# Kernel tuning notes

Measured on AMD Instinct MI355X. Metric: run time of the kernel, lower is better.

Reference implementation:

```python
import jax, jax.numpy as jnp
import numpy as np

H = 64  # hidden_dim

def _lstm_dir(x, Wih, Whh, bih, bhh, reverse):
    # x: [B, T, D]; Wih: [4H, D]; Whh: [4H, H]; PyTorch gate order i,f,g,o
    B, T, _ = x.shape
    if reverse:
        x = x[:, ::-1, :]
    # Precompute input contribution to all gates: [B, T, 4H]
    xg = jnp.einsum('btd,gd->btg', x, Wih) + (bih + bhh)
    h0 = jnp.zeros((B, H), x.dtype)
    c0 = jnp.zeros((B, H), x.dtype)

    def step(carry, xg_t):
        h, c = carry
        g = xg_t + h @ Whh.T  # [B, 4H]
        i, f, gg, o = jnp.split(g, 4, axis=-1)
        i = jax.nn.sigmoid(i)
        f = jax.nn.sigmoid(f)
        gg = jnp.tanh(gg)
        o = jax.nn.sigmoid(o)
        c = f * c + i * gg
        h = o * jnp.tanh(c)
        return (h, c), h

    (hT, cT), hs = jax.lax.scan(step, (h0, c0), jnp.swapaxes(xg, 0, 1))
    hs = jnp.swapaxes(hs, 0, 1)  # [B, T, H]
    if reverse:
        hs = hs[:, ::-1, :]
    return hs, hT

def _forward(x, Wih_l0_f, Whh_l0_f, bih_l0_f, bhh_l0_f,
             Wih_l0_b, Whh_l0_b, bih_l0_b, bhh_l0_b,
             Wih_l1_f, Whh_l1_f, bih_l1_f, bhh_l1_f,
             Wih_l1_b, Whh_l1_b, bih_l1_b, bhh_l1_b,
             fc1_W, fc1_b, fc2_W, fc2_b):
    xt = jnp.transpose(x, (0, 2, 1))  # [B, 512, 3]
    # Layer 0 (bidirectional)
    hs_f, _ = _lstm_dir(xt, Wih_l0_f, Whh_l0_f, bih_l0_f, bhh_l0_f, False)
    hs_b, _ = _lstm_dir(xt, Wih_l0_b, Whh_l0_b, bih_l0_b, bhh_l0_b, True)
    y0 = jnp.concatenate([hs_f, hs_b], axis=-1)  # [B, 512, 2H]
    # (inter-layer dropout is identity in eval mode)
    # Layer 1 (bidirectional); only final hidden states needed
    _, hT_f = _lstm_dir(y0, Wih_l1_f, Whh_l1_f, bih_l1_f, bhh_l1_f, False)
    _, hT_b = _lstm_dir(y0, Wih_l1_b, Whh_l1_b, bih_l1_b, bhh_l1_b, True)
    h = jnp.concatenate([hT_f, hT_b], axis=-1)  # [B, 2H]
    h = jax.nn.relu(h @ fc1_W.T + fc1_b)
    return h @ fc2_W.T + fc2_b  # [B, num_classes]

def setup_inputs() -> dict:
    key = jax.random.key(0)
    ks = iter(jax.random.split(key, 32))
    B, T, C = 1024, 512, 3
    d = {}
    d['x'] = jax.random.normal(next(ks), (B, C, T), dtype=jnp.float32)
    # PyTorch-style bias init: forget-gate bias = 1, rest 0
    bias = jnp.zeros((4 * H,), jnp.float32).at[H:2 * H].set(1.0)
    for layer, din in [(0, C), (1, 2 * H)]:
        for dirn in ['f', 'b']:
            d[f'Wih_l{layer}_{dirn}'] = jax.random.normal(next(ks), (4 * H, din), dtype=jnp.float32) * 0.1
            d[f'Whh_l{layer}_{dirn}'] = jax.random.normal(next(ks), (4 * H, H), dtype=jnp.float32) * 0.1
            d[f'bih_l{layer}_{dirn}'] = bias
            d[f'bhh_l{layer}_{dirn}'] = jnp.zeros((4 * H,), jnp.float32)
    d['fc1_W'] = jax.random.normal(next(ks), (H, 2 * H), dtype=jnp.float32) * 0.1
    d['fc1_b'] = jnp.zeros((H,), jnp.float32)
    d['fc2_W'] = jax.random.normal(next(ks), (2, H), dtype=jnp.float32) * 0.1
    d['fc2_b'] = jnp.zeros((2,), jnp.float32)
    return d

def reference(x, Wih_l0_f, Whh_l0_f, bih_l0_f, bhh_l0_f,
              Wih_l0_b, Whh_l0_b, bih_l0_b, bhh_l0_b,
              Wih_l1_f, Whh_l1_f, bih_l1_f, bhh_l1_f,
              Wih_l1_b, Whh_l1_b, bih_l1_b, bhh_l1_b,
              fc1_W, fc1_b, fc2_W, fc2_b):
    return _forward(x, Wih_l0_f, Whh_l0_f, bih_l0_f, bhh_l0_f,
                    Wih_l0_b, Whh_l0_b, bih_l0_b, bhh_l0_b,
                    Wih_l1_f, Whh_l1_f, bih_l1_f, bhh_l1_f,
                    Wih_l1_b, Whh_l1_b, bih_l1_b, bhh_l1_b,
                    fc1_W, fc1_b, fc2_W, fc2_b)
```

## Files before the change

kernel.cpp:

```cpp
#include <hip/hip_runtime.h>
#include <stdint.h>

typedef __attribute__((ext_vector_type(8))) short short8;
typedef __attribute__((ext_vector_type(4))) float f32x4;

#define TT 512
#define LSTR 136
#define XS 516

static __device__ __forceinline__ uint32_t f2bf_u(float f){
  union { float f; uint32_t u; } v; v.f = f;
  return (v.u + 0x7fffu + ((v.u >> 16) & 1u)) >> 16;
}
static __device__ __forceinline__ short8 w8f32(const float* p){
  float4 a = *(const float4*)p;
  float4 b = *(const float4*)(p + 4);
  short8 r;
  r[0] = (short)f2bf_u(a.x); r[1] = (short)f2bf_u(a.y);
  r[2] = (short)f2bf_u(a.z); r[3] = (short)f2bf_u(a.w);
  r[4] = (short)f2bf_u(b.x); r[5] = (short)f2bf_u(b.y);
  r[6] = (short)f2bf_u(b.z); r[7] = (short)f2bf_u(b.w);
  return r;
}
static __device__ __forceinline__ float sigx(float x){
  float e = __builtin_amdgcn_exp2f(-1.442695040888963f * x);
  return __builtin_amdgcn_rcpf(1.f + e);
}
static __device__ __forceinline__ float tanhx(float x){
  float e = __builtin_amdgcn_exp2f(-2.885390081777927f * x);
  return fmaf(__builtin_amdgcn_rcpf(1.f + e), 2.f, -1.f);
}
static __device__ __forceinline__ void lds_barrier(){
  asm volatile("s_waitcnt lgkmcnt(0)" ::: "memory");
  __builtin_amdgcn_s_barrier();
}
#define MF(A,B,C) __builtin_amdgcn_mfma_f32_16x16x32_bf16((A),(B),(C),0,0,0)

#define NONLIN_WRITE(A0V, A1V, P1) do { \
    float g0_ = sel0 ? (A0V)[0] : (A1V)[0]; \
    float g1_ = sel0 ? (A0V)[1] : (A1V)[1]; \
    float g2_ = sel0 ? (A0V)[2] : (A1V)[2]; \
    float g3_ = sel0 ? (A0V)[3] : (A1V)[3]; \
    float ii_ = sigx(g0_), ff_ = sigx(g1_), gg_ = tanhx(g2_), oo_ = sigx(g3_); \
    c = fmaf(ff_, c, ii_ * gg_); \
    h = oo_ * tanhx(c); \
    sZ[P1][m8][colw] = (unsigned short)f2bf_u(h); \
  } while(0)

__global__ __launch_bounds__(512, 2) void lstm_l0(
    const float* __restrict__ x,
    const float* __restrict__ Wih_f, const float* __restrict__ Whh_f,
    const float* __restrict__ bih_f, const float* __restrict__ bhh_f,
    const float* __restrict__ Wih_b, const float* __restrict__ Whh_b,
    const float* __restrict__ bih_b, const float* __restrict__ bhh_b,
    unsigned short* __restrict__ y0)
{
  const int tid = threadIdx.x;
  const int wv = tid >> 6, lane = tid & 63;
  const int quad = lane >> 4, m16 = lane & 15;
  const int dir = blockIdx.y;
  const int bbase = blockIdx.x * 8;
  const float* Wih = dir ? Wih_b : Wih_f;
  const float* Whh = dir ? Whh_b : Whh_f;
  const float* bih = dir ? bih_b : bih_f;
  const float* bhh = dir ? bhh_b : bhh_f;

  __shared__ __align__(16) unsigned short sZ[2][8][LSTR];
  __shared__ __align__(16) float sX[24 * XS];

  short8 aH[2][2];
  f32x4 biasv[2];
  float Wf[2][4][3];
  const int gm = (m16 & 3) * 64 + (m16 >> 2);
  #pragma unroll
  for (int i = 0; i < 2; i++){
    const int rt = 2 * wv + i;
    const int g = gm + 4 * rt;
    aH[i][0] = w8f32(Whh + g * 64 + quad * 8);
    aH[i][1] = w8f32(Whh + g * 64 + 32 + quad * 8);
    const int gu = 4 * rt + quad;
    #pragma unroll
    for (int r = 0; r < 4; r++){
      biasv[i][r] = bih[r * 64 + gu] + bhh[r * 64 + gu];
      #pragma unroll
      for (int d = 0; d < 3; d++) Wf[i][r][d] = Wih[(r * 64 + gu) * 3 + d];
    }
  }

  for (int idx = tid; idx < 2 * 8 * LSTR; idx += 512)
    ((unsigned short*)sZ)[idx] = 0;
  for (int i4 = tid; i4 < 3072; i4 += 512){
    const int row = i4 >> 7, t4 = (i4 & 127) * 4;
    *(float4*)&sX[row * XS + t4] = *(const float4*)(x + (size_t)bbase * 1536 + row * 512 + t4);
  }
  __syncthreads();

  const int m8 = m16 & 7;
  const int xrow = 3 * m8;
  const bool sel0 = (m16 < 8);
  const int colw = 8 * wv + quad + ((m16 >> 3) << 2);
  float c = 0.f, h = 0.f;

#define FFCOMP(F0, F1, TIDX) do { \
    float x0_ = sX[xrow * XS + (TIDX)]; \
    float x1_ = sX[(xrow + 1) * XS + (TIDX)]; \
    float x2_ = sX[(xrow + 2) * XS + (TIDX)]; \
    _Pragma("unroll") \
    for (int r_ = 0; r_ < 4; r_++){ \
      F0[r_] = fmaf(Wf[0][r_][2], x2_, fmaf(Wf[0][r_][1], x1_, fmaf(Wf[0][r_][0], x0_, biasv[0][r_]))); \
      F1[r_] = fmaf(Wf[1][r_][2], x2_, fmaf(Wf[1][r_][1], x1_, fmaf(Wf[1][r_][0], x0_, biasv[1][r_]))); \
    } \
  } while(0)

  f32x4 FBa0, FBa1, FBb0, FBb1;
  {
    const int t0_ = dir ? (TT - 1) : 0;
    FFCOMP(FBa0, FBa1, t0_);
  }

#define L0STEP(S, P, FC0, FC1, FN0, FN1) do { \
    const int p1_ = (P) ^ 1; \
    short8 bh0 = *(const short8*)&sZ[P][m8][     quad * 8]; \
    short8 bh1 = *(const short8*)&sZ[P][m8][32 + quad * 8]; \
    if (lane < 8 && (S) > 0){ \
      const int tprev = dir ? (TT - (S)) : ((S) - 1); \
      uint4 v_ = *(const uint4*)&sZ[P][wv][lane * 8]; \
      *(uint4*)(y0 + ((size_t)(bbase + wv) * TT + tprev) * 128 + dir * 64 + lane * 8) = v_; \
    } \
    f32x4 A0 = MF(aH[0][0], bh0, FC0); \
    f32x4 A1 = MF(aH[1][0], bh0, FC1); \
    A0 = MF(aH[0][1], bh1, A0); \
    A1 = MF(aH[1][1], bh1, A1); \
    { int sn_ = (S) + 1; if (sn_ > TT - 1) sn_ = TT - 1; \
      const int tn_ = dir ? (TT - 1 - sn_) : sn_; \
      FFCOMP(FN0, FN1, tn_); \
    } \
    __builtin_amdgcn_sched_barrier(0); \
    NONLIN_WRITE(A0, A1, p1_); \
    __builtin_amdgcn_sched_barrier(0); \
    lds_barrier(); \
  } while(0)

  for (int s = 0; s < TT; s += 4){
    L0STEP(s,     0, FBa0, FBa1, FBb0, FBb1);
    L0STEP(s + 1, 1, FBb0, FBb1, FBa0, FBa1);
    L0STEP(s + 2, 0, FBa0, FBa1, FBb0, FBb1);
    L0STEP(s + 3, 1, FBb0, FBb1, FBa0, FBa1);
  }
#undef L0STEP
#undef FFCOMP

  if (lane < 8){
    const int tl = dir ? 0 : (TT - 1);
    uint4 v = *(const uint4*)&sZ[0][wv][lane * 8];
    *(uint4*)(y0 + ((size_t)(bbase + wv) * TT + tl) * 128 + dir * 64 + lane * 8) = v;
  }
}

__global__ __launch_bounds__(512, 2) void lstm_l1(
    const unsigned short* __restrict__ y0,
    const float* __restrict__ Wih_f, const float* __restrict__ Whh_f,
    const float* __restrict__ bih_f, const float* __restrict__ bhh_f,
    const float* __restrict__ Wih_b, const float* __restrict__ Whh_b,
    const float* __restrict__ bih_b, const float* __restrict__ bhh_b,
    float* __restrict__ hT)
{
  const int tid = threadIdx.x;
  const int wv = tid >> 6, lane = tid & 63;
  const int quad = lane >> 4, m16 = lane & 15;
  const int dir = blockIdx.y;
  const int bbase = blockIdx.x * 8;
  const float* Wih = dir ? Wih_b : Wih_f;
  const float* Whh = dir ? Whh_b : Whh_f;
  const float* bih = dir ? bih_b : bih_f;
  const float* bhh = dir ? bhh_b : bhh_f;

  __shared__ __align__(16) unsigned short sZ[2][8][LSTR];
  __shared__ __align__(16) unsigned short sY[4][8][LSTR];

  short8 aY[2][4], aH[2][2];
  f32x4 biasv[2];
  const int gm = (m16 & 3) * 64 + (m16 >> 2);
  #pragma unroll
  for (int i = 0; i < 2; i++){
    const int rt = 2 * wv + i;
    const int g = gm + 4 * rt;
    #pragma unroll
    for (int kt = 0; kt < 4; kt++) aY[i][kt] = w8f32(Wih + g * 128 + kt * 32 + quad * 8);
    aH[i][0] = w8f32(Whh + g * 64 + quad * 8);
    aH[i][1] = w8f32(Whh + g * 64 + 32 + quad * 8);
    const int gu = 4 * rt + quad;
    #pragma unroll
    for (int r = 0; r < 4; r++) biasv[i][r] = bih[r * 64 + gu] + bhh[r * 64 + gu];
  }

  for (int idx = tid; idx < 2 * 8 * LSTR; idx += 512)
    ((unsigned short*)sZ)[idx] = 0;

  const bool stager = (lane < 16);
  const size_t sgbase = (size_t)(bbase + wv) * TT * 128 + (size_t)lane * 8;
  float4 hA = make_float4(0.f,0.f,0.f,0.f), hB = make_float4(0.f,0.f,0.f,0.f);
  if (stager){
    const int t0 = dir ? (TT-1) : 0, t1 = dir ? (TT-2) : 1, t2 = dir ? (TT-3) : 2;
    const int t3 = dir ? (TT-4) : 3, t4 = dir ? (TT-5) : 4;
    float4 v0 = *(const float4*)(y0 + sgbase + (size_t)t0 * 128);
    float4 v1 = *(const float4*)(y0 + sgbase + (size_t)t1 * 128);
    float4 v2 = *(const float4*)(y0 + sgbase + (size_t)t2 * 128);
    hA = *(const float4*)(y0 + sgbase + (size_t)t3 * 128);
    hB = *(const float4*)(y0 + sgbase + (size_t)t4 * 128);
    *(float4*)&sY[0][wv][lane * 8] = v0;
    *(float4*)&sY[1][wv][lane * 8] = v1;
    *(float4*)&sY[2][wv][lane * 8] = v2;
  }
  __syncthreads();

  const int m8 = m16 & 7;
  const bool sel0 = (m16 < 8);
  const int colw = 8 * wv + quad + ((m16 >> 3) << 2);
  float c = 0.f, h = 0.f;

  f32x4 FBa0, FBa1, FBb0, FBb1;
  {
    short8 by0 = *(const short8*)&sY[0][m8][     quad * 8];
    short8 by1 = *(const short8*)&sY[0][m8][32 + quad * 8];
    short8 by2 = *(const short8*)&sY[0][m8][64 + quad * 8];
    short8 by3 = *(const short8*)&sY[0][m8][96 + quad * 8];
    FBa0 = MF(aY[0][0], by0, biasv[0]);
    FBa1 = MF(aY[1][0], by0, biasv[1]);
    FBa0 = MF(aY[0][1], by1, FBa0);  FBa1 = MF(aY[1][1], by1, FBa1);
    FBa0 = MF(aY[0][2], by2, FBa0);  FBa1 = MF(aY[1][2], by2, FBa1);
    FBa0 = MF(aY[0][3], by3, FBa0);  FBa1 = MF(aY[1][3], by3, FBa1);
  }

#define L1STEP(S, P, SLOT, WSLOT, HOLD, FC0, FC1, FN0, FN1) do { \
    const int p1_ = (P) ^ 1; \
    short8 bh0 = *(const short8*)&sZ[P][m8][     quad * 8]; \
    short8 bh1 = *(const short8*)&sZ[P][m8][32 + quad * 8]; \
    short8 by0 = *(const short8*)&sY[SLOT][m8][     quad * 8]; \
    short8 by1 = *(const short8*)&sY[SLOT][m8][32 + quad * 8]; \
    short8 by2 = *(const short8*)&sY[SLOT][m8][64 + quad * 8]; \
    short8 by3 = *(const short8*)&sY[SLOT][m8][96 + quad * 8]; \
    f32x4 A0 = MF(aH[0][0], bh0, FC0); \
    f32x4 A1 = MF(aH[1][0], bh0, FC1); \
    A0 = MF(aH[0][1], bh1, A0); \
    A1 = MF(aH[1][1], bh1, A1); \
    FN0 = MF(aY[0][0], by0, biasv[0]); \
    FN1 = MF(aY[1][0], by0, biasv[1]); \
    FN0 = MF(aY[0][1], by1, FN0);  FN1 = MF(aY[1][1], by1, FN1); \
    FN0 = MF(aY[0][2], by2, FN0);  FN1 = MF(aY[1][2], by2, FN1); \
    FN0 = MF(aY[0][3], by3, FN0);  FN1 = MF(aY[1][3], by3, FN1); \
    __builtin_amdgcn_sched_barrier(0); \
    NONLIN_WRITE(A0, A1, p1_); \
    if ((S) == TT - 1){ \
      hT[(size_t)(bbase + m8) * 128 + dir * 64 + colw] = h; \
    } \
    if (stager){ \
      *(float4*)&sY[WSLOT][wv][lane * 8] = HOLD; \
      int sg_ = (S) + 5; if (sg_ > TT - 1) sg_ = TT - 1; \
      const int tg_ = dir ? (TT - 1 - sg_) : sg_; \
      HOLD = *(const float4*)(y0 + sgbase + (size_t)tg_ * 128); \
    } \
    __builtin_amdgcn_sched_barrier(0); \
    lds_barrier(); \
  } while(0)

  for (int s = 0; s < TT; s += 4){
    L1STEP(s,     0, 1, 3, hA, FBa0, FBa1, FBb0, FBb1);
    L1STEP(s + 1, 1, 2, 0, hB, FBb0, FBb1, FBa0, FBa1);
    L1STEP(s + 2, 0, 3, 1, hA, FBa0, FBa1, FBb0, FBb1);
    L1STEP(s + 3, 1, 0, 2, hB, FBb0, FBb1, FBa0, FBa1);
  }
#undef L1STEP
}

__global__ __launch_bounds__(256, 1) void fc_kernel(
    const float* __restrict__ hT,
    const float* __restrict__ w1, const float* __restrict__ b1,
    const float* __restrict__ w2, const float* __restrict__ b2,
    float* __restrict__ out)
{
  __shared__ float sh[4][64];
  const int wave = threadIdx.x >> 6, lane = threadIdx.x & 63;
  const int b = blockIdx.x * 4 + wave;
  float acc = b1[lane];
  const float* hrow = hT + (size_t)b * 128;
  #pragma unroll
  for (int k = 0; k < 128; k += 4){
    float4 h4 = *(const float4*)(hrow + k);
    float4 w4 = *(const float4*)(w1 + lane * 128 + k);
    acc = fmaf(w4.x, h4.x, acc);
    acc = fmaf(w4.y, h4.y, acc);
    acc = fmaf(w4.z, h4.z, acc);
    acc = fmaf(w4.w, h4.w, acc);
  }
  sh[wave][lane] = fmaxf(acc, 0.f);
  __syncthreads();
  if (lane < 2){
    float a = b2[lane];
    #pragma unroll
    for (int k = 0; k < 64; k++) a = fmaf(w2[lane * 64 + k], sh[wave][k], a);
    out[(size_t)b * 2 + lane] = a;
  }
}

extern "C" void kernel_launch(void* const* d_in, const int* in_sizes, int n_in,
                              void* d_out, int out_size, void* d_ws, size_t ws_size,
                              hipStream_t stream){
  (void)in_sizes; (void)n_in; (void)out_size; (void)ws_size;
  const float* x     = (const float*)d_in[0];
  const float* Wih0f = (const float*)d_in[1];
  const float* Whh0f = (const float*)d_in[2];
  const float* bih0f = (const float*)d_in[3];
  const float* bhh0f = (const float*)d_in[4];
  const float* Wih0b = (const float*)d_in[5];
  const float* Whh0b = (const float*)d_in[6];
  const float* bih0b = (const float*)d_in[7];
  const float* bhh0b = (const float*)d_in[8];
  const float* Wih1f = (const float*)d_in[9];
  const float* Whh1f = (const float*)d_in[10];
  const float* bih1f = (const float*)d_in[11];
  const float* bhh1f = (const float*)d_in[12];
  const float* Wih1b = (const float*)d_in[13];
  const float* Whh1b = (const float*)d_in[14];
  const float* bih1b = (const float*)d_in[15];
  const float* bhh1b = (const float*)d_in[16];
  const float* fc1W  = (const float*)d_in[17];
  const float* fc1b  = (const float*)d_in[18];
  const float* fc2W  = (const float*)d_in[19];
  const float* fc2b  = (const float*)d_in[20];
  float* out = (float*)d_out;

  unsigned short* y0 = (unsigned short*)d_ws;
  float* hT = (float*)((char*)d_ws + (size_t)1024 * TT * 128 * 2);

  dim3 grid(128, 2), block(512);
  lstm_l0<<<grid, block, 0, stream>>>(x, Wih0f, Whh0f, bih0f, bhh0f,
                                      Wih0b, Whh0b, bih0b, bhh0b, y0);
  lstm_l1<<<grid, block, 0, stream>>>(y0, Wih1f, Whh1f, bih1f, bhh1f,
                                      Wih1b, Whh1b, bih1b, bhh1b, hT);
  fc_kernel<<<dim3(256), dim3(256), 0, stream>>>(hT, fc1W, fc1b, fc2W, fc2b, out);
}
```

Before: 530.6 us.

## Restructure layer-0 LSTM to 4 batches per block with 256 threads

Layer-0 kernel now handles 4 batch rows per block with 4 waves instead of 8 rows with 8 waves, doubling the grid to 512 blocks. Each wave issues 4 MFMA tiles per half-K instead of 2, and the input projection is added after the MFMA rather than seeded into the accumulator. Each lane selects its gate values from the 4 tiles by its copy index. The goal is more blocks across the CUs and a shorter per-step barrier over fewer waves on the serial recurrence, at the cost of redundant MFMA work on duplicated batch columns.

After: 517.1 us. -2.5%, faster.

```diff
diff --git a/kernel.cpp b/kernel.cpp
--- a/kernel.cpp
+++ b/kernel.cpp
@@ -36,18 +36,7 @@
 }
 #define MF(A,B,C) __builtin_amdgcn_mfma_f32_16x16x32_bf16((A),(B),(C),0,0,0)
 
-#define NONLIN_WRITE(A0V, A1V, P1) do { \
-    float g0_ = sel0 ? (A0V)[0] : (A1V)[0]; \
-    float g1_ = sel0 ? (A0V)[1] : (A1V)[1]; \
-    float g2_ = sel0 ? (A0V)[2] : (A1V)[2]; \
-    float g3_ = sel0 ? (A0V)[3] : (A1V)[3]; \
-    float ii_ = sigx(g0_), ff_ = sigx(g1_), gg_ = tanhx(g2_), oo_ = sigx(g3_); \
-    c = fmaf(ff_, c, ii_ * gg_); \
-    h = oo_ * tanhx(c); \
-    sZ[P1][m8][colw] = (unsigned short)f2bf_u(h); \
-  } while(0)
-
-__global__ __launch_bounds__(512, 2) void lstm_l0(
+__global__ __launch_bounds__(256, 2) void lstm_l0(
     const float* __restrict__ x,
     const float* __restrict__ Wih_f, const float* __restrict__ Whh_f,
     const float* __restrict__ bih_f, const float* __restrict__ bhh_f,
@@ -59,103 +48,127 @@
   const int wv = tid >> 6, lane = tid & 63;
   const int quad = lane >> 4, m16 = lane & 15;
   const int dir = blockIdx.y;
-  const int bbase = blockIdx.x * 8;
+  const int bbase = blockIdx.x * 4;
   const float* Wih = dir ? Wih_b : Wih_f;
   const float* Whh = dir ? Whh_b : Whh_f;
   const float* bih = dir ? bih_b : bih_f;
   const float* bhh = dir ? bhh_b : bhh_f;
 
-  __shared__ __align__(16) unsigned short sZ[2][8][LSTR];
-  __shared__ __align__(16) float sX[24 * XS];
-
-  short8 aH[2][2];
-  f32x4 biasv[2];
-  float Wf[2][4][3];
+  __shared__ __align__(16) unsigned short sZ[2][4][LSTR];
+  __shared__ __align__(16) float sX[12 * XS];
+
+  const int copy = m16 >> 2;
+  const int batch = m16 & 3;
+  const int unit = 16 * wv + 4 * copy + quad;
+  const bool selA = (copy & 1) != 0;
+  const bool selB = (copy & 2) != 0;
+
+  short8 aH[4][2];
   const int gm = (m16 & 3) * 64 + (m16 >> 2);
   #pragma unroll
-  for (int i = 0; i < 2; i++){
-    const int rt = 2 * wv + i;
-    const int g = gm + 4 * rt;
-    aH[i][0] = w8f32(Whh + g * 64 + quad * 8);
-    aH[i][1] = w8f32(Whh + g * 64 + 32 + quad * 8);
-    const int gu = 4 * rt + quad;
+  for (int k = 0; k < 4; k++){
+    const int g = gm + 4 * (4 * wv + k);
+    aH[k][0] = w8f32(Whh + g * 64 + quad * 8);
+    aH[k][1] = w8f32(Whh + g * 64 + 32 + quad * 8);
+  }
+  float Wf[4][3];
+  f32x4 biasF;
+  #pragma unroll
+  for (int r = 0; r < 4; r++){
+    biasF[r] = bih[r * 64 + unit] + bhh[r * 64 + unit];
     #pragma unroll
-    for (int r = 0; r < 4; r++){
-      biasv[i][r] = bih[r * 64 + gu] + bhh[r * 64 + gu];
-      #pragma unroll
-      for (int d = 0; d < 3; d++) Wf[i][r][d] = Wih[(r * 64 + gu) * 3 + d];
-    }
-  }
-
-  for (int idx = tid; idx < 2 * 8 * LSTR; idx += 512)
+    for (int d = 0; d < 3; d++) Wf[r][d] = Wih[(r * 64 + unit) * 3 + d];
+  }
+
+  for (int idx = tid; idx < 2 * 4 * LSTR; idx += 256)
     ((unsigned short*)sZ)[idx] = 0;
-  for (int i4 = tid; i4 < 3072; i4 += 512){
+  for (int i4 = tid; i4 < 1536; i4 += 256){
     const int row = i4 >> 7, t4 = (i4 & 127) * 4;
     *(float4*)&sX[row * XS + t4] = *(const float4*)(x + (size_t)bbase * 1536 + row * 512 + t4);
   }
   __syncthreads();
 
-  const int m8 = m16 & 7;
-  const int xrow = 3 * m8;
-  const bool sel0 = (m16 < 8);
-  const int colw = 8 * wv + quad + ((m16 >> 3) << 2);
+  const int xrow = 3 * batch;
   float c = 0.f, h = 0.f;
-
-#define FFCOMP(F0, F1, TIDX) do { \
+  const f32x4 z4 = {0.f, 0.f, 0.f, 0.f};
+
+#define FFCOMP(F, TIDX) do { \
     float x0_ = sX[xrow * XS + (TIDX)]; \
     float x1_ = sX[(xrow + 1) * XS + (TIDX)]; \
     float x2_ = sX[(xrow + 2) * XS + (TIDX)]; \
     _Pragma("unroll") \
-    for (int r_ = 0; r_ < 4; r_++){ \
-      F0[r_] = fmaf(Wf[0][r_][2], x2_, fmaf(Wf[0][r_][1], x1_, fmaf(Wf[0][r_][0], x0_, biasv[0][r_]))); \
-      F1[r_] = fmaf(Wf[1][r_][2], x2_, fmaf(Wf[1][r_][1], x1_, fmaf(Wf[1][r_][0], x0_, biasv[1][r_]))); \
-    } \
+    for (int r_ = 0; r_ < 4; r_++) \
+      F[r_] = fmaf(Wf[r_][2], x2_, fmaf(Wf[r_][1], x1_, fmaf(Wf[r_][0], x0_, biasF[r_]))); \
   } while(0)
 
-  f32x4 FBa0, FBa1, FBb0, FBb1;
+  f32x4 FBa, FBb;
   {
     const int t0_ = dir ? (TT - 1) : 0;
-    FFCOMP(FBa0, FBa1, t0_);
-  }
-
-#define L0STEP(S, P, FC0, FC1, FN0, FN1) do { \
+    FFCOMP(FBa, t0_);
+  }
+
+#define L0STEP(S, P, FC, FN) do { \
     const int p1_ = (P) ^ 1; \
-    short8 bh0 = *(const short8*)&sZ[P][m8][     quad * 8]; \
-    short8 bh1 = *(const short8*)&sZ[P][m8][32 + quad * 8]; \
-    if (lane < 8 && (S) > 0){ \
+    short8 bh0 = *(const short8*)&sZ[P][batch][     quad * 8]; \
+    short8 bh1 = *(const short8*)&sZ[P][batch][32 + quad * 8]; \
+    if (wv == 3 && lane < 32 && (S) > 0){ \
       const int tprev = dir ? (TT - (S)) : ((S) - 1); \
-      uint4 v_ = *(const uint4*)&sZ[P][wv][lane * 8]; \
-      *(uint4*)(y0 + ((size_t)(bbase + wv) * TT + tprev) * 128 + dir * 64 + lane * 8) = v_; \
-    } \
-    f32x4 A0 = MF(aH[0][0], bh0, FC0); \
-    f32x4 A1 = MF(aH[1][0], bh0, FC1); \
-    A0 = MF(aH[0][1], bh1, A0); \
-    A1 = MF(aH[1][1], bh1, A1); \
+      const int br_ = lane >> 3, cc_ = lane & 7; \
+      uint4 v_ = *(const uint4*)&sZ[P][br_][cc_ * 8]; \
+      *(uint4*)(y0 + ((size_t)(bbase + br_) * TT + tprev) * 128 + dir * 64 + cc_ * 8) = v_; \
+    } \
+    f32x4 C0 = MF(aH[0][0], bh0, z4); \
+    f32x4 C1 = MF(aH[1][0], bh0, z4); \
+    f32x4 C2 = MF(aH[2][0], bh0, z4); \
+    f32x4 C3 = MF(aH[3][0], bh0, z4); \
+    C0 = MF(aH[0][1], bh1, C0); \
+    C1 = MF(aH[1][1], bh1, C1); \
+    C2 = MF(aH[2][1], bh1, C2); \
+    C3 = MF(aH[3][1], bh1, C3); \
     { int sn_ = (S) + 1; if (sn_ > TT - 1) sn_ = TT - 1; \
       const int tn_ = dir ? (TT - 1 - sn_) : sn_; \
-      FFCOMP(FN0, FN1, tn_); \
+      FFCOMP(FN, tn_); \
     } \
     __builtin_amdgcn_sched_barrier(0); \
-    NONLIN_WRITE(A0, A1, p1_); \
+    { \
+      float g0_ = (selB ? (selA ? C3[0] : C2[0]) : (selA ? C1[0] : C0[0])) + FC[0]; \
+      float g1_ = (selB ? (selA ? C3[1] : C2[1]) : (selA ? C1[1] : C0[1])) + FC[1]; \
+      float g2_ = (selB ? (selA ? C3[2] : C2[2]) : (selA ? C1[2] : C0[2])) + FC[2]; \
+      float g3_ = (selB ? (selA ? C3[3] : C2[3]) : (selA ? C1[3] : C0[3])) + FC[3]; \
+      float ii_ = sigx(g0_), ff_ = sigx(g1_), gg_ = tanhx(g2_), oo_ = sigx(g3_); \
+      c = fmaf(ff_, c, ii_ * gg_); \
+      h = oo_ * tanhx(c); \
+      sZ[p1_][batch][unit] = (unsigned short)f2bf_u(h); \
+    } \
     __builtin_amdgcn_sched_barrier(0); \
     lds_barrier(); \
   } while(0)
 
-  for (int s = 0; s < TT; s += 4){
-    L0STEP(s,     0, FBa0, FBa1, FBb0, FBb1);
-    L0STEP(s + 1, 1, FBb0, FBb1, FBa0, FBa1);
-    L0STEP(s + 2, 0, FBa0, FBa1, FBb0, FBb1);
-    L0STEP(s + 3, 1, FBb0, FBb1, FBa0, FBa1);
+  for (int s = 0; s < TT; s += 2){
+    L0STEP(s,     0, FBa, FBb);
+    L0STEP(s + 1, 1, FBb, FBa);
   }
 #undef L0STEP
 #undef FFCOMP
 
-  if (lane < 8){
+  if (wv == 3 && lane < 32){
     const int tl = dir ? 0 : (TT - 1);
-    uint4 v = *(const uint4*)&sZ[0][wv][lane * 8];
-    *(uint4*)(y0 + ((size_t)(bbase + wv) * TT + tl) * 128 + dir * 64 + lane * 8) = v;
-  }
-}
+    const int br = lane >> 3, cc = lane & 7;
+    uint4 v = *(const uint4*)&sZ[0][br][cc * 8];
+    *(uint4*)(y0 + ((size_t)(bbase + br) * TT + tl) * 128 + dir * 64 + cc * 8) = v;
+  }
+}
+
+#define NONLIN_WRITE(A0V, A1V, P1) do { \
+    float g0_ = sel0 ? (A0V)[0] : (A1V)[0]; \
+    float g1_ = sel0 ? (A0V)[1] : (A1V)[1]; \
+    float g2_ = sel0 ? (A0V)[2] : (A1V)[2]; \
+    float g3_ = sel0 ? (A0V)[3] : (A1V)[3]; \
+    float ii_ = sigx(g0_), ff_ = sigx(g1_), gg_ = tanhx(g2_), oo_ = sigx(g3_); \
+    c = fmaf(ff_, c, ii_ * gg_); \
+    h = oo_ * tanhx(c); \
+    sZ[P1][m8][colw] = (unsigned short)f2bf_u(h); \
+  } while(0)
 
 __global__ __launch_bounds__(512, 2) void lstm_l1(
     const unsigned short* __restrict__ y0,
@@ -333,10 +346,9 @@
   unsigned short* y0 = (unsigned short*)d_ws;
   float* hT = (float*)((char*)d_ws + (size_t)1024 * TT * 128 * 2);
 
-  dim3 grid(128, 2), block(512);
-  lstm_l0<<<grid, block, 0, stream>>>(x, Wih0f, Whh0f, bih0f, bhh0f,
-                                      Wih0b, Whh0b, bih0b, bhh0b, y0);
-  lstm_l1<<<grid, block, 0, stream>>>(y0, Wih1f, Whh1f, bih1f, bhh1f,
-                                      Wih1b, Whh1b, bih1b, bhh1b, hT);
+  lstm_l0<<<dim3(256, 2), dim3(256), 0, stream>>>(x, Wih0f, Whh0f, bih0f, bhh0f,
+                                                  Wih0b, Whh0b, bih0b, bhh0b, y0);
+  lstm_l1<<<dim3(128, 2), dim3(512), 0, stream>>>(y0, Wih1f, Whh1f, bih1f, bhh1f,
+                                                  Wih1b, Whh1b, bih1b, bhh1b, hT);
   fc_kernel<<<dim3(256), dim3(256), 0, stream>>>(hT, fc1W, fc1b, fc2W, fc2b, out);
 }
```
